# Kernel tuning notes

Measured on AMD Instinct MI355X. Metric: run time of the kernel, lower is better.

Reference implementation:

```python
import jax, jax.numpy as jnp
import numpy as np

EPS = 1e-15
N_NODES = 20000
N_EDGES = 640000
FEAT = 128
N_RBF = 20
CUTOFF = 5.0


def setup_inputs() -> dict:
    key = jax.random.key(0)
    ks = jax.random.split(key, 10)
    s_j = jax.random.normal(ks[0], (N_NODES, FEAT), jnp.float32)
    v_j = jax.random.normal(ks[1], (N_NODES, FEAT, 3), jnp.float32)
    r_ij = jax.random.normal(ks[2], (N_EDGES, 3), jnp.float32)
    nbrs = jax.random.randint(ks[3], (N_EDGES, 2), 0, N_NODES, jnp.int64)
    # InvariantDense: Dense(F->F, swish) then Dense(F->3F)
    W1 = jax.random.normal(ks[4], (FEAT, FEAT), jnp.float32) / np.sqrt(FEAT)
    b1 = jnp.zeros((FEAT,), jnp.float32)
    W2 = jax.random.normal(ks[5], (FEAT, 3 * FEAT), jnp.float32) / np.sqrt(FEAT)
    b2 = jnp.zeros((3 * FEAT,), jnp.float32)
    # DistanceEmbed dense: Dense(n_rbf -> 3F)
    Wd = jax.random.normal(ks[6], (N_RBF, 3 * FEAT), jnp.float32) / np.sqrt(N_RBF)
    bd = jnp.zeros((3 * FEAT,), jnp.float32)
    return {"s_j": s_j, "v_j": v_j, "r_ij": r_ij, "nbrs": nbrs,
            "W1": W1, "b1": b1, "W2": W2, "b2": b2, "Wd": Wd, "bd": bd}


def reference(s_j, v_j, r_ij, nbrs, W1, b1, W2, b2, Wd, bd):
    N, F = s_j.shape
    # preprocess_r
    dist = jnp.sqrt(jnp.sum(r_ij ** 2 + EPS, axis=-1))          # [E]
    unit = r_ij / dist[:, None]                                  # [E,3]
    # InvariantDense on nodes (dense before gather, as in torch code)
    phi_node = jax.nn.silu(s_j @ W1 + b1) @ W2 + b2              # [N,3F]
    phi = phi_node[nbrs[:, 1]]                                   # [E,3F]
    # PaiNN radial basis: sin(n*pi*d/cutoff)/d, n=1..n_rbf
    k = jnp.arange(1, N_RBF + 1, dtype=dist.dtype) * (np.pi / CUTOFF)  # [n_rbf]
    rbf = jnp.sin(dist[:, None] * k[None, :]) / dist[:, None]    # [E,n_rbf]
    # cosine cutoff envelope
    env = 0.5 * (jnp.cos(np.pi * dist / CUTOFF) + 1.0)
    env = jnp.where(dist < CUTOFF, env, 0.0)                     # [E]
    w_s = (rbf @ Wd + bd) * env[:, None]                         # [E,3F]
    inv = (phi * w_s).reshape(-1, 3, F)                          # [E,3,F]
    split0 = inv[:, 0, :][:, :, None]                            # [E,F,1]
    split1 = inv[:, 1, :]                                        # [E,F]
    split2 = inv[:, 2, :][:, :, None]                            # [E,F,1]
    delta_v_ij = split2 * unit[:, None, :] + split0 * v_j[nbrs[:, 1]]  # [E,F,3]
    idx = nbrs[:, 0]
    delta_s_i = jax.ops.segment_sum(split1, idx, num_segments=N)      # [N,F]
    delta_v_i = jax.ops.segment_sum(delta_v_ij, idx, num_segments=N)  # [N,F,3]
    return (delta_s_i, delta_v_i)
```

## Files before the change

kernel.cpp:

```cpp
#include <hip/hip_runtime.h>
#include <hip/hip_bf16.h>
#include <math.h>

typedef __hip_bfloat16 bf16;

#define FEAT 128
#define NRBF 20
#define CUTOFF_F 5.0f
#define KSCALE 0.62831853071795864769f

__device__ __forceinline__ float b2f(bf16 x) { return __bfloat162float(x); }
__device__ __forceinline__ bf16 f2b(float x) { return __float2bfloat16(x); }

template<int F32>
__device__ __forceinline__ float LD(const void* p, size_t i) {
    if (F32) return ((const float*)p)[i];
    return b2f(((const bf16*)p)[i]);
}
template<int F32>
__device__ __forceinline__ void ST(void* p, size_t i, float v) {
    if (F32) ((float*)p)[i] = v;
    else ((bf16*)p)[i] = f2b(v);
}

__device__ __forceinline__ int get_dst(const int* nb, int e, int is64) {
    return is64 ? nb[4 * e] : nb[2 * e];
}
__device__ __forceinline__ int get_src(const int* nb, int e, int is64) {
    return is64 ? nb[4 * e + 2] : nb[2 * e + 1];
}
__device__ __forceinline__ int clampi(int v, int n) {
    return v < 0 ? 0 : (v >= n ? n - 1 : v);
}

__global__ void init_kernel(const void* __restrict__ s_ptr, const int* __restrict__ nbrs32,
                            int nE, int* __restrict__ flags, int* __restrict__ counts, int nN) {
    int t = blockIdx.x * blockDim.x + threadIdx.x;
    if (t < nN) counts[t] = 0;
    if (t == 0) {
        const unsigned* u = (const unsigned*)s_ptr;
        int hits = 0;
        for (int i = 0; i < 64; ++i) {
            unsigned ef = (u[i] >> 7) & 0xFF;
            hits += (ef >= 110 && ef <= 135) ? 1 : 0;
        }
        flags[0] = (hits < 32) ? 1 : 0;
        int lim = 2 * nE; if (lim > 128) lim = 128;
        int allz = 1;
        for (int i = 1; i < lim; i += 2) allz &= (nbrs32[i] == 0);
        flags[1] = allz;
    }
}

__global__ void hist_kernel(const int* __restrict__ nbrs, const int* __restrict__ flags,
                            int* __restrict__ counts, int nE, int nN) {
    int e = blockIdx.x * blockDim.x + threadIdx.x;
    if (e < nE) {
        int d = clampi(get_dst(nbrs, e, flags[1]), nN);
        atomicAdd(&counts[d], 1);
    }
}

__global__ __launch_bounds__(1024) void scan_kernel(const int* __restrict__ counts,
        int* __restrict__ offsets, int* __restrict__ cursor, int nN) {
    __shared__ int part[1024];
    const int t = threadIdx.x;
    const int chunk = (nN + 1023) / 1024;
    const int base = t * chunk;
    int local[32];
    int sum = 0;
    for (int c = 0; c < chunk && c < 32; ++c) {
        int idx = base + c;
        int v = (idx < nN) ? counts[idx] : 0;
        local[c] = v;
        sum += v;
    }
    part[t] = sum;
    __syncthreads();
    for (int off = 1; off < 1024; off <<= 1) {
        int add = (t >= off) ? part[t - off] : 0;
        __syncthreads();
        part[t] += add;
        __syncthreads();
    }
    int run = part[t] - sum;
    for (int c = 0; c < chunk && c < 32; ++c) {
        int idx = base + c;
        if (idx < nN) { offsets[idx] = run; cursor[idx] = run; run += local[c]; }
    }
    if (t == 1023) offsets[nN] = part[1023];
}

__global__ __launch_bounds__(384) void prep_kernel(const void* __restrict__ Wd,
        const void* __restrict__ bd, float* __restrict__ WdT, const int* __restrict__ flags) {
    const int c = threadIdx.x;
    const int F32 = flags[0];
    if (F32) {
        for (int k = 0; k < NRBF; ++k) WdT[c * 24 + k] = ((const float*)Wd)[k * 384 + c];
        WdT[c * 24 + 20] = ((const float*)bd)[c];
    } else {
        for (int k = 0; k < NRBF; ++k) WdT[c * 24 + k] = b2f(((const bf16*)Wd)[k * 384 + c]);
        WdT[c * 24 + 20] = b2f(((const bf16*)bd)[c]);
    }
    WdT[c * 24 + 21] = 0.f; WdT[c * 24 + 22] = 0.f; WdT[c * 24 + 23] = 0.f;
}

template<int F32, int MODEA>
__device__ void pre_scatter_body(const void* __restrict__ r_ij, const int* __restrict__ nbrs,
        int is64, int* __restrict__ cursor, int* __restrict__ src_ids,
        float4* __restrict__ u_env, int* __restrict__ pos_of_e, float* __restrict__ gbuf,
        int e, int nE, int nN) {
    const int d = clampi(get_dst(nbrs, e, is64), nN);
    const int j = clampi(get_src(nbrs, e, is64), nN);
    int pos = atomicAdd(&cursor[d], 1);
    pos = clampi(pos, nE);
    src_ids[pos] = j;

    const float rx = LD<F32>(r_ij, (size_t)3 * e + 0);
    const float ry = LD<F32>(r_ij, (size_t)3 * e + 1);
    const float rz = LD<F32>(r_ij, (size_t)3 * e + 2);
    const float d2   = rx * rx + ry * ry + rz * rz + 3e-15f;
    const float invd = rsqrtf(d2);
    const float dd   = d2 * invd;
    const float x  = dd * KSCALE;
    const float c1 = F32 ? cosf(x) : __cosf(x);
    const float env = (dd < CUTOFF_F) ? (0.5f * (c1 + 1.0f)) : 0.0f;
    u_env[pos] = make_float4(rx * invd, ry * invd, rz * invd, env);

    if (MODEA) {
        pos_of_e[e] = pos;
    } else {
        const float s1 = F32 ? sinf(x) : __sinf(x);
        const float scale = invd * env;
        const float tc = 2.0f * c1;
        float skm2 = 0.f, skm1 = s1;
        float* g = gbuf + (size_t)pos * NRBF;
        g[0] = s1 * scale;
        #pragma unroll
        for (int k = 1; k < NRBF; ++k) {
            const float sk = fmaf(tc, skm1, -skm2);
            g[k] = sk * scale;
            skm2 = skm1; skm1 = sk;
        }
    }
}

__global__ __launch_bounds__(256) void pre_scatter_kernel(const void* r_ij, const int* nbrs,
        const int* __restrict__ flags, int* cursor, int* src_ids, float4* u_env,
        int* pos_of_e, float* gbuf, int nE, int nN, int modeA) {
    int e = blockIdx.x * blockDim.x + threadIdx.x;
    if (e >= nE) return;
    const int F32 = flags[0], is64 = flags[1];
    if (modeA) {
        if (F32) pre_scatter_body<1,1>(r_ij, nbrs, is64, cursor, src_ids, u_env, pos_of_e, gbuf, e, nE, nN);
        else     pre_scatter_body<0,1>(r_ij, nbrs, is64, cursor, src_ids, u_env, pos_of_e, gbuf, e, nE, nN);
    } else {
        if (F32) pre_scatter_body<1,0>(r_ij, nbrs, is64, cursor, src_ids, u_env, pos_of_e, gbuf, e, nE, nN);
        else     pre_scatter_body<0,0>(r_ij, nbrs, is64, cursor, src_ids, u_env, pos_of_e, gbuf, e, nE, nN);
    }
}

template<int F32>
__device__ void gemm_body(const void* __restrict__ s_j, const void* __restrict__ W1,
                          const void* __restrict__ b1, const void* __restrict__ W2,
                          const void* __restrict__ b2v, bf16* __restrict__ phi, int nN,
                          int packed) {
    __shared__ float sl[8][FEAT];
    __shared__ float hl[8][FEAT];
    const int t = threadIdx.x;
    const int n0 = blockIdx.x * 8;
    for (int idx = t; idx < 8 * FEAT; idx += 384) {
        int n = idx >> 7, k = idx & 127;
        int row = n0 + n;
        sl[n][k] = (row < nN) ? LD<F32>(s_j, (size_t)row * FEAT + k) : 0.f;
    }
    __syncthreads();
    for (int idx = t; idx < 8 * FEAT; idx += 384) {
        int n = idx >> 7, f = idx & 127;
        float a = 0.f;
        #pragma unroll 4
        for (int k = 0; k < FEAT; ++k) a = fmaf(sl[n][k], LD<F32>(W1, (size_t)k * FEAT + f), a);
        a += LD<F32>(b1, f);
        float sg = F32 ? (1.0f / (1.0f + expf(-a))) : (1.0f / (1.0f + __expf(-a)));
        hl[n][f] = a * sg;
    }
    __syncthreads();
    float acc[8] = {};
    #pragma unroll 4
    for (int k = 0; k < FEAT; ++k) {
        const float w = LD<F32>(W2, (size_t)k * 384 + t);
        #pragma unroll
        for (int n = 0; n < 8; ++n) acc[n] = fmaf(hl[n][k], w, acc[n]);
    }
    const float bb = LD<F32>(b2v, t);
    const int fch  = t & 127;
    const int comp = t >> 7;
    #pragma unroll
    for (int n = 0; n < 8; ++n) {
        int row = n0 + n;
        if (row < nN) {
            if (packed) phi[((size_t)row * FEAT + fch) * 8 + comp] = f2b(acc[n] + bb);
            else        phi[(size_t)row * 384 + t] = f2b(acc[n] + bb);
        }
    }
}

__global__ __launch_bounds__(384) void gemm_node_kernel(const void* s_j, const void* W1,
        const void* b1, const void* W2, const void* b2v, bf16* phi,
        const int* __restrict__ flags, int nN, int packed) {
    if (flags[0]) gemm_body<1>(s_j, W1, b1, W2, b2v, phi, nN, packed);
    else          gemm_body<0>(s_j, W1, b1, W2, b2v, phi, nN, packed);
}

__global__ __launch_bounds__(256) void pack_v_kernel(const void* __restrict__ v_j,
        bf16* __restrict__ rec, const int* __restrict__ flags, int nN) {
    int t = blockIdx.x * blockDim.x + threadIdx.x;
    if (t >= nN * FEAT) return;
    float vx, vy, vz;
    if (flags[0]) {
        const float* v = (const float*)v_j;
        vx = v[(size_t)3 * t + 0];
        vy = v[(size_t)3 * t + 1];
        vz = v[(size_t)3 * t + 2];
    } else {
        const bf16* v = (const bf16*)v_j;
        vx = b2f(v[(size_t)3 * t + 0]);
        vy = b2f(v[(size_t)3 * t + 1]);
        vz = b2f(v[(size_t)3 * t + 2]);
    }
    bf16* d = rec + (size_t)t * 8;
    union { bf16 b[2]; unsigned u; } p01;
    p01.b[0] = f2b(vx); p01.b[1] = f2b(vy);
    *(unsigned*)(d + 4) = p01.u;
    d[6] = f2b(vz);
}

template<int F32>
__device__ void pre_ws_body(const void* __restrict__ r_ij, const float* __restrict__ WdT,
        const int* __restrict__ pos_of_e, bf16* __restrict__ ws_w, int e) {
    const float rx = LD<F32>(r_ij, (size_t)3 * e + 0);
    const float ry = LD<F32>(r_ij, (size_t)3 * e + 1);
    const float rz = LD<F32>(r_ij, (size_t)3 * e + 2);
    const float d2   = rx * rx + ry * ry + rz * rz + 3e-15f;
    const float invd = rsqrtf(d2);
    const float dd   = d2 * invd;
    const float x  = dd * KSCALE;
    const float s1 = F32 ? sinf(x) : __sinf(x);
    const float c1 = F32 ? cosf(x) : __cosf(x);
    const float env = (dd < CUTOFF_F) ? (0.5f * (c1 + 1.0f)) : 0.0f;
    const float scale = invd * env;
    float gk[NRBF];
    const float tc = 2.0f * c1;
    float skm2 = 0.f, skm1 = s1;
    gk[0] = s1 * scale;
    #pragma unroll
    for (int k = 1; k < NRBF; ++k) {
        const float sk = fmaf(tc, skm1, -skm2);
        gk[k] = sk * scale;
        skm2 = skm1; skm1 = sk;
    }
    const int pos = pos_of_e[e];
    bf16* dst = ws_w + (size_t)pos * 384;
    for (int c0 = 0; c0 < 384; c0 += 4) {
        float r[4];
        #pragma unroll
        for (int u = 0; u < 4; ++u) {
            const float* w = WdT + (size_t)(c0 + u) * 24;
            float acc = w[20] * env;
            #pragma unroll
            for (int k = 0; k < NRBF; ++k) acc = fmaf(gk[k], w[k], acc);
            r[u] = acc;
        }
        union { bf16 b[4]; uint2 u2; } pk;
        pk.b[0] = f2b(r[0]); pk.b[1] = f2b(r[1]); pk.b[2] = f2b(r[2]); pk.b[3] = f2b(r[3]);
        *(uint2*)(dst + c0) = pk.u2;
    }
}

__global__ __launch_bounds__(256) void pre_ws_kernel(const void* r_ij,
        const float* __restrict__ WdT, const int* __restrict__ pos_of_e,
        bf16* __restrict__ ws_w, const int* __restrict__ flags, int nE) {
    int e = blockIdx.x * blockDim.x + threadIdx.x;
    if (e >= nE) return;
    if (flags[0]) pre_ws_body<1>(r_ij, WdT, pos_of_e, ws_w, e);
    else          pre_ws_body<0>(r_ij, WdT, pos_of_e, ws_w, e);
}

template<int F32>
__device__ void msg_a_body(const bf16* __restrict__ ws_w, const bf16* __restrict__ phi,
        const void* __restrict__ v_j, const int* __restrict__ src_ids,
        const float4* __restrict__ u_env, const int* __restrict__ offsets,
        void* __restrict__ out, int nE, int nN) {
    const int i = blockIdx.x;
    const int f = threadIdx.x;
    int start = offsets[i];
    int end   = offsets[i + 1];
    if (start < 0) start = 0;
    if (end > nE) end = nE;

    float ds = 0.f, dv0 = 0.f, dv1 = 0.f, dv2 = 0.f;

    #pragma unroll 2
    for (int p = start; p < end; ++p) {
        const int j = src_ids[p];
        const float4 ue = u_env[p];
        const bf16* wr = ws_w + (size_t)p * 384;
        const float w0 = b2f(wr[f]);
        const float w1 = b2f(wr[FEAT + f]);
        const float w2 = b2f(wr[2 * FEAT + f]);
        const bf16* ph = phi + (size_t)j * 384;
        const float p0 = b2f(ph[f]);
        const float p1 = b2f(ph[FEAT + f]);
        const float p2 = b2f(ph[2 * FEAT + f]);
        const float vx = LD<F32>(v_j, ((size_t)j * FEAT + f) * 3 + 0);
        const float vy = LD<F32>(v_j, ((size_t)j * FEAT + f) * 3 + 1);
        const float vz = LD<F32>(v_j, ((size_t)j * FEAT + f) * 3 + 2);
        const float i0 = w0 * p0;
        const float i1 = w1 * p1;
        const float i2 = w2 * p2;
        ds += i1;
        dv0 = fmaf(i2, ue.x, fmaf(i0, vx, dv0));
        dv1 = fmaf(i2, ue.y, fmaf(i0, vy, dv1));
        dv2 = fmaf(i2, ue.z, fmaf(i0, vz, dv2));
    }

    ST<F32>(out, (size_t)i * FEAT + f, ds);
    const size_t ob = (size_t)nN * FEAT + ((size_t)i * FEAT + f) * 3;
    ST<F32>(out, ob + 0, dv0);
    ST<F32>(out, ob + 1, dv1);
    ST<F32>(out, ob + 2, dv2);
}

__global__ __launch_bounds__(128) void msg_a_kernel(const bf16* ws_w, const bf16* phi,
        const void* v_j, const int* src_ids, const float4* u_env, const int* offsets,
        const int* __restrict__ flags, void* out, int nE, int nN) {
    if (flags[0]) msg_a_body<1>(ws_w, phi, v_j, src_ids, u_env, offsets, out, nE, nN);
    else          msg_a_body<0>(ws_w, phi, v_j, src_ids, u_env, offsets, out, nE, nN);
}

template<int F32>
__device__ void msg_c_body(const float* __restrict__ WdT, const bf16* __restrict__ rec,
        const float* __restrict__ gbuf, const int* __restrict__ src_ids,
        const float4* __restrict__ u_env, const int* __restrict__ offsets,
        void* __restrict__ out, int nE, int nN) {
    const int i = blockIdx.x;
    const int f = threadIdx.x;
    int start = offsets[i];
    int end   = offsets[i + 1];
    if (start < 0) start = 0;
    if (end > nE) end = nE;

    const float* w0p = WdT + (size_t)f * 24;
    const float* w1p = WdT + (size_t)(f + FEAT) * 24;
    const float* w2p = WdT + (size_t)(f + 2 * FEAT) * 24;

    float ds = 0.f, dv0 = 0.f, dv1 = 0.f, dv2 = 0.f;

    for (int p = start; p < end; ++p) {
        const int j = src_ids[p];
        const float4 ue = u_env[p];
        const float* g = gbuf + (size_t)p * NRBF;
        float t0 = 0.f, t1 = 0.f, t2 = 0.f;
        #pragma unroll
        for (int k = 0; k < NRBF; ++k) {
            const float gk = g[k];
            t0 = fmaf(gk, w0p[k], t0);
            t1 = fmaf(gk, w1p[k], t1);
            t2 = fmaf(gk, w2p[k], t2);
        }
        const float w0 = fmaf(w0p[20], ue.w, t0);
        const float w1 = fmaf(w1p[20], ue.w, t1);
        const float w2 = fmaf(w2p[20], ue.w, t2);

        const uint4 rv = *(const uint4*)(rec + ((size_t)j * FEAT + f) * 8);
        const float p0 = __uint_as_float(rv.x << 16);
        const float p1 = __uint_as_float(rv.x & 0xffff0000u);
        const float p2 = __uint_as_float(rv.y << 16);
        const float vx = __uint_as_float(rv.z << 16);
        const float vy = __uint_as_float(rv.z & 0xffff0000u);
        const float vz = __uint_as_float(rv.w << 16);

        const float i0 = w0 * p0;
        const float i1 = w1 * p1;
        const float i2 = w2 * p2;
        ds += i1;
        dv0 = fmaf(i2, ue.x, fmaf(i0, vx, dv0));
        dv1 = fmaf(i2, ue.y, fmaf(i0, vy, dv1));
        dv2 = fmaf(i2, ue.z, fmaf(i0, vz, dv2));
    }

    ST<F32>(out, (size_t)i * FEAT + f, ds);
    const size_t ob = (size_t)nN * FEAT + ((size_t)i * FEAT + f) * 3;
    ST<F32>(out, ob + 0, dv0);
    ST<F32>(out, ob + 1, dv1);
    ST<F32>(out, ob + 2, dv2);
}

__global__ __launch_bounds__(128) void msg_c_kernel(const float* WdT, const bf16* rec,
        const float* gbuf, const int* src_ids, const float4* u_env, const int* offsets,
        const int* __restrict__ flags, void* out, int nE, int nN) {
    if (flags[0]) msg_c_body<1>(WdT, rec, gbuf, src_ids, u_env, offsets, out, nE, nN);
    else          msg_c_body<0>(WdT, rec, gbuf, src_ids, u_env, offsets, out, nE, nN);
}

template<int F32>
__device__ void msg_b_body(const void* __restrict__ v_j, const void* __restrict__ Wd,
        const void* __restrict__ bd, const bf16* __restrict__ phi,
        const float* __restrict__ gbuf, const int* __restrict__ src_ids,
        const float4* __restrict__ u_env, const int* __restrict__ offsets,
        void* __restrict__ out, int nE, int nN) {
    const int i = blockIdx.x;
    const int f = threadIdx.x;

    float wd0[NRBF], wd1[NRBF], wd2[NRBF];
    #pragma unroll
    for (int k = 0; k < NRBF; ++k) {
        wd0[k] = LD<F32>(Wd, (size_t)k * 384 + f);
        wd1[k] = LD<F32>(Wd, (size_t)k * 384 + FEAT + f);
        wd2[k] = LD<F32>(Wd, (size_t)k * 384 + 2 * FEAT + f);
    }
    const float bd0 = LD<F32>(bd, f);
    const float bd1 = LD<F32>(bd, FEAT + f);
    const float bd2 = LD<F32>(bd, 2 * FEAT + f);

    int start = offsets[i];
    int end   = offsets[i + 1];
    if (start < 0) start = 0;
    if (end > nE) end = nE;

    float ds = 0.f, dv0 = 0.f, dv1 = 0.f, dv2 = 0.f;

    for (int p = start; p < end; ++p) {
        const int j = src_ids[p];
        const float4 ue = u_env[p];
        const float* g = gbuf + (size_t)p * NRBF;
        float t0 = 0.f, t1 = 0.f, t2 = 0.f;
        #pragma unroll
        for (int k = 0; k < NRBF; ++k) {
            const float gk = g[k];
            t0 = fmaf(gk, wd0[k], t0);
            t1 = fmaf(gk, wd1[k], t1);
            t2 = fmaf(gk, wd2[k], t2);
        }
        const float w0 = fmaf(bd0, ue.w, t0);
        const float w1 = fmaf(bd1, ue.w, t1);
        const float w2 = fmaf(bd2, ue.w, t2);

        const bf16* ph = phi + (size_t)j * 384;
        const float p0 = b2f(ph[f]);
        const float p1 = b2f(ph[FEAT + f]);
        const float p2 = b2f(ph[2 * FEAT + f]);
        const float vx = LD<F32>(v_j, ((size_t)j * FEAT + f) * 3 + 0);
        const float vy = LD<F32>(v_j, ((size_t)j * FEAT + f) * 3 + 1);
        const float vz = LD<F32>(v_j, ((size_t)j * FEAT + f) * 3 + 2);

        const float i0 = w0 * p0;
        const float i1 = w1 * p1;
        const float i2 = w2 * p2;
        ds += i1;
        dv0 = fmaf(i2, ue.x, fmaf(i0, vx, dv0));
        dv1 = fmaf(i2, ue.y, fmaf(i0, vy, dv1));
        dv2 = fmaf(i2, ue.z, fmaf(i0, vz, dv2));
    }

    ST<F32>(out, (size_t)i * FEAT + f, ds);
    const size_t ob = (size_t)nN * FEAT + ((size_t)i * FEAT + f) * 3;
    ST<F32>(out, ob + 0, dv0);
    ST<F32>(out, ob + 1, dv1);
    ST<F32>(out, ob + 2, dv2);
}

__global__ __launch_bounds__(128) void msg_b_kernel(const void* v_j, const void* Wd,
        const void* bd, const bf16* phi, const float* gbuf, const int* src_ids,
        const float4* u_env, const int* offsets, const int* __restrict__ flags,
        void* out, int nE, int nN) {
    if (flags[0]) msg_b_body<1>(v_j, Wd, bd, phi, gbuf, src_ids, u_env, offsets, out, nE, nN);
    else          msg_b_body<0>(v_j, Wd, bd, phi, gbuf, src_ids, u_env, offsets, out, nE, nN);
}

extern "C" void kernel_launch(void* const* d_in, const int* in_sizes, int n_in,
                              void* d_out, int out_size, void* d_ws, size_t ws_size,
                              hipStream_t stream) {
    const void* s_j  = d_in[0];
    const void* v_j  = d_in[1];
    const void* r_ij = d_in[2];
    const int*  nbrs = (const int*)d_in[3];
    const void* W1   = d_in[4];
    const void* b1   = d_in[5];
    const void* W2   = d_in[6];
    const void* b2   = d_in[7];
    const void* Wd   = d_in[8];
    const void* bd   = d_in[9];

    const int nN = out_size / (4 * FEAT);
    const int nE = in_sizes[2] / 3;

    char* ws = (char*)d_ws;
    size_t off = 0;
    auto alloc = [&](size_t bytes) -> void* {
        void* p = ws + off;
        off = (off + bytes + 255) & ~(size_t)255;
        return p;
    };
    int*    flags    = (int*)alloc(16);
    int*    counts   = (int*)alloc((size_t)nN * 4);
    int*    offsets  = (int*)alloc(((size_t)nN + 1) * 4);
    int*    cursor   = (int*)alloc((size_t)nN * 4);
    int*    src_ids  = (int*)alloc((size_t)nE * 4);
    float4* u_env    = (float4*)alloc((size_t)nE * 16);
    float*  WdT      = (float*)alloc((size_t)384 * 24 * 4);
    const size_t base = off;

    size_t offA = base;
    int*  pos_of_e = (int*)(ws + offA);  offA += ((size_t)nE * 4 + 255) & ~(size_t)255;
    bf16* phiA     = (bf16*)(ws + offA); offA += ((size_t)nN * 384 * 2 + 255) & ~(size_t)255;
    bf16* ws_w     = (bf16*)(ws + offA); offA += (size_t)nE * 384 * 2;
    size_t offC = base;
    float* gbufC = (float*)(ws + offC);  offC += ((size_t)nE * NRBF * 4 + 255) & ~(size_t)255;
    bf16*  rec   = (bf16*)(ws + offC);   offC += (size_t)nN * FEAT * 8 * 2;
    size_t offB = base;
    float* gbufB = (float*)(ws + offB);  offB += ((size_t)nE * NRBF * 4 + 255) & ~(size_t)255;
    bf16*  phiB  = (bf16*)(ws + offB);   offB += (size_t)nN * 384 * 2;

    const int modeA = (ws_size >= offA) ? 1 : 0;
    const int modeC = (!modeA && ws_size >= offC) ? 1 : 0;

    init_kernel<<<(nN + 255) / 256, 256, 0, stream>>>(s_j, nbrs, nE, flags, counts, nN);
    hist_kernel<<<(nE + 255) / 256, 256, 0, stream>>>(nbrs, flags, counts, nE, nN);
    scan_kernel<<<1, 1024, 0, stream>>>(counts, offsets, cursor, nN);
    prep_kernel<<<1, 384, 0, stream>>>(Wd, bd, WdT, flags);

    pre_scatter_kernel<<<(nE + 255) / 256, 256, 0, stream>>>(
        r_ij, nbrs, flags, cursor, src_ids, u_env, pos_of_e, gbufC, nE, nN, modeA);

    if (modeA) {
        gemm_node_kernel<<<(nN + 7) / 8, 384, 0, stream>>>(s_j, W1, b1, W2, b2, phiA, flags, nN, 0);
        pre_ws_kernel<<<(nE + 255) / 256, 256, 0, stream>>>(r_ij, WdT, pos_of_e, ws_w, flags, nE);
        msg_a_kernel<<<nN, 128, 0, stream>>>(ws_w, phiA, v_j, src_ids, u_env, offsets,
                                             flags, d_out, nE, nN);
    } else if (modeC) {
        gemm_node_kernel<<<(nN + 7) / 8, 384, 0, stream>>>(s_j, W1, b1, W2, b2, rec, flags, nN, 1);
        pack_v_kernel<<<((nN * FEAT) + 255) / 256, 256, 0, stream>>>(v_j, rec, flags, nN);
        msg_c_kernel<<<nN, 128, 0, stream>>>(WdT, rec, gbufC, src_ids, u_env, offsets,
                                             flags, d_out, nE, nN);
    } else {
        gemm_node_kernel<<<(nN + 7) / 8, 384, 0, stream>>>(s_j, W1, b1, W2, b2, phiB, flags, nN, 0);
        msg_b_kernel<<<nN, 128, 0, stream>>>(v_j, Wd, bd, phiB, gbufC, src_ids, u_env,
                                             offsets, flags, d_out, nE, nN);
    }
}
```

Measured before the change: 546.6 us.

## Split scatter into index pass and sorted-order RBF finalize; preload Wd in registers

In mode C the scatter pass now records only the source id and the original edge index for each sorted position. A new finalize kernel walks positions in sorted order and computes u_env and the RBF vector, writing them with contiguous float4 stores instead of scattered 80-byte writes. The message kernel loads its Wd rows into registers once and reads gbuf as float4, with launch bounds set to 128 threads and 2 blocks. The cost is an extra kernel launch, a gathered read of r_ij, and an extra nE-sized index buffer in the workspace, which may change which mode is selected.

After: 559.7 us. +2.4%, slower.

```diff
diff --git a/kernel.cpp b/kernel.cpp
--- a/kernel.cpp
+++ b/kernel.cpp
@@ -105,16 +105,21 @@
     WdT[c * 24 + 21] = 0.f; WdT[c * 24 + 22] = 0.f; WdT[c * 24 + 23] = 0.f;
 }
 
-template<int F32, int MODEA>
+template<int F32, int MODE>
 __device__ void pre_scatter_body(const void* __restrict__ r_ij, const int* __restrict__ nbrs,
         int is64, int* __restrict__ cursor, int* __restrict__ src_ids,
         float4* __restrict__ u_env, int* __restrict__ pos_of_e, float* __restrict__ gbuf,
-        int e, int nE, int nN) {
+        int* __restrict__ edge_of_pos, int e, int nE, int nN) {
     const int d = clampi(get_dst(nbrs, e, is64), nN);
     const int j = clampi(get_src(nbrs, e, is64), nN);
     int pos = atomicAdd(&cursor[d], 1);
     pos = clampi(pos, nE);
     src_ids[pos] = j;
+
+    if (MODE == 2) {
+        edge_of_pos[pos] = e;
+        return;
+    }
 
     const float rx = LD<F32>(r_ij, (size_t)3 * e + 0);
     const float ry = LD<F32>(r_ij, (size_t)3 * e + 1);
@@ -127,7 +132,7 @@
     const float env = (dd < CUTOFF_F) ? (0.5f * (c1 + 1.0f)) : 0.0f;
     u_env[pos] = make_float4(rx * invd, ry * invd, rz * invd, env);
 
-    if (MODEA) {
+    if (MODE == 1) {
         pos_of_e[e] = pos;
     } else {
         const float s1 = F32 ? sinf(x) : __sinf(x);
@@ -147,17 +152,62 @@
 
 __global__ __launch_bounds__(256) void pre_scatter_kernel(const void* r_ij, const int* nbrs,
         const int* __restrict__ flags, int* cursor, int* src_ids, float4* u_env,
-        int* pos_of_e, float* gbuf, int nE, int nN, int modeA) {
+        int* pos_of_e, float* gbuf, int* edge_of_pos, int nE, int nN, int mode) {
     int e = blockIdx.x * blockDim.x + threadIdx.x;
     if (e >= nE) return;
     const int F32 = flags[0], is64 = flags[1];
-    if (modeA) {
-        if (F32) pre_scatter_body<1,1>(r_ij, nbrs, is64, cursor, src_ids, u_env, pos_of_e, gbuf, e, nE, nN);
-        else     pre_scatter_body<0,1>(r_ij, nbrs, is64, cursor, src_ids, u_env, pos_of_e, gbuf, e, nE, nN);
+    if (mode == 2) {
+        if (F32) pre_scatter_body<1,2>(r_ij, nbrs, is64, cursor, src_ids, u_env, pos_of_e, gbuf, edge_of_pos, e, nE, nN);
+        else     pre_scatter_body<0,2>(r_ij, nbrs, is64, cursor, src_ids, u_env, pos_of_e, gbuf, edge_of_pos, e, nE, nN);
+    } else if (mode == 1) {
+        if (F32) pre_scatter_body<1,1>(r_ij, nbrs, is64, cursor, src_ids, u_env, pos_of_e, gbuf, edge_of_pos, e, nE, nN);
+        else     pre_scatter_body<0,1>(r_ij, nbrs, is64, cursor, src_ids, u_env, pos_of_e, gbuf, edge_of_pos, e, nE, nN);
     } else {
-        if (F32) pre_scatter_body<1,0>(r_ij, nbrs, is64, cursor, src_ids, u_env, pos_of_e, gbuf, e, nE, nN);
-        else     pre_scatter_body<0,0>(r_ij, nbrs, is64, cursor, src_ids, u_env, pos_of_e, gbuf, e, nE, nN);
-    }
+        if (F32) pre_scatter_body<1,0>(r_ij, nbrs, is64, cursor, src_ids, u_env, pos_of_e, gbuf, edge_of_pos, e, nE, nN);
+        else     pre_scatter_body<0,0>(r_ij, nbrs, is64, cursor, src_ids, u_env, pos_of_e, gbuf, edge_of_pos, e, nE, nN);
+    }
+}
+
+template<int F32>
+__device__ void finalize_body(const void* __restrict__ r_ij, const int* __restrict__ edge_of_pos,
+        float4* __restrict__ u_env, float* __restrict__ gbuf, int t, int nE) {
+    const int e = clampi(edge_of_pos[t], nE);
+    const float rx = LD<F32>(r_ij, (size_t)3 * e + 0);
+    const float ry = LD<F32>(r_ij, (size_t)3 * e + 1);
+    const float rz = LD<F32>(r_ij, (size_t)3 * e + 2);
+    const float d2   = rx * rx + ry * ry + rz * rz + 3e-15f;
+    const float invd = rsqrtf(d2);
+    const float dd   = d2 * invd;
+    const float x  = dd * KSCALE;
+    const float c1 = F32 ? cosf(x) : __cosf(x);
+    const float s1 = F32 ? sinf(x) : __sinf(x);
+    const float env = (dd < CUTOFF_F) ? (0.5f * (c1 + 1.0f)) : 0.0f;
+    u_env[t] = make_float4(rx * invd, ry * invd, rz * invd, env);
+
+    const float scale = invd * env;
+    const float tc = 2.0f * c1;
+    float g[NRBF];
+    float skm2 = 0.f, skm1 = s1;
+    g[0] = s1 * scale;
+    #pragma unroll
+    for (int k = 1; k < NRBF; ++k) {
+        const float sk = fmaf(tc, skm1, -skm2);
+        g[k] = sk * scale;
+        skm2 = skm1; skm1 = sk;
+    }
+    float4* gd = (float4*)(gbuf + (size_t)t * NRBF);
+    #pragma unroll
+    for (int q = 0; q < 5; ++q)
+        gd[q] = make_float4(g[4*q], g[4*q+1], g[4*q+2], g[4*q+3]);
+}
+
+__global__ __launch_bounds__(256) void finalize_kernel(const void* r_ij,
+        const int* __restrict__ edge_of_pos, float4* __restrict__ u_env,
+        float* __restrict__ gbuf, const int* __restrict__ flags, int nE) {
+    int t = blockIdx.x * blockDim.x + threadIdx.x;
+    if (t >= nE) return;
+    if (flags[0]) finalize_body<1>(r_ij, edge_of_pos, u_env, gbuf, t, nE);
+    else          finalize_body<0>(r_ij, edge_of_pos, u_env, gbuf, t, nE);
 }
 
 template<int F32>
@@ -350,27 +400,36 @@
     if (start < 0) start = 0;
     if (end > nE) end = nE;
 
-    const float* w0p = WdT + (size_t)f * 24;
-    const float* w1p = WdT + (size_t)(f + FEAT) * 24;
-    const float* w2p = WdT + (size_t)(f + 2 * FEAT) * 24;
+    const float4* wq0 = (const float4*)(WdT + (size_t)f * 24);
+    const float4* wq1 = (const float4*)(WdT + (size_t)(f + FEAT) * 24);
+    const float4* wq2 = (const float4*)(WdT + (size_t)(f + 2 * FEAT) * 24);
+    float4 A0[5], A1[5], A2[5];
+    #pragma unroll
+    for (int q = 0; q < 5; ++q) { A0[q] = wq0[q]; A1[q] = wq1[q]; A2[q] = wq2[q]; }
+    const float B0 = WdT[(size_t)f * 24 + 20];
+    const float B1 = WdT[(size_t)(f + FEAT) * 24 + 20];
+    const float B2 = WdT[(size_t)(f + 2 * FEAT) * 24 + 20];
 
     float ds = 0.f, dv0 = 0.f, dv1 = 0.f, dv2 = 0.f;
 
     for (int p = start; p < end; ++p) {
         const int j = src_ids[p];
         const float4 ue = u_env[p];
-        const float* g = gbuf + (size_t)p * NRBF;
+        const float4* g4 = (const float4*)(gbuf + (size_t)p * NRBF);
         float t0 = 0.f, t1 = 0.f, t2 = 0.f;
         #pragma unroll
-        for (int k = 0; k < NRBF; ++k) {
-            const float gk = g[k];
-            t0 = fmaf(gk, w0p[k], t0);
-            t1 = fmaf(gk, w1p[k], t1);
-            t2 = fmaf(gk, w2p[k], t2);
+        for (int q = 0; q < 5; ++q) {
+            const float4 gq = g4[q];
+            t0 = fmaf(gq.x, A0[q].x, t0); t0 = fmaf(gq.y, A0[q].y, t0);
+            t0 = fmaf(gq.z, A0[q].z, t0); t0 = fmaf(gq.w, A0[q].w, t0);
+            t1 = fmaf(gq.x, A1[q].x, t1); t1 = fmaf(gq.y, A1[q].y, t1);
+            t1 = fmaf(gq.z, A1[q].z, t1); t1 = fmaf(gq.w, A1[q].w, t1);
+            t2 = fmaf(gq.x, A2[q].x, t2); t2 = fmaf(gq.y, A2[q].y, t2);
+            t2 = fmaf(gq.z, A2[q].z, t2); t2 = fmaf(gq.w, A2[q].w, t2);
         }
-        const float w0 = fmaf(w0p[20], ue.w, t0);
-        const float w1 = fmaf(w1p[20], ue.w, t1);
-        const float w2 = fmaf(w2p[20], ue.w, t2);
+        const float w0 = fmaf(B0, ue.w, t0);
+        const float w1 = fmaf(B1, ue.w, t1);
+        const float w2 = fmaf(B2, ue.w, t2);
 
         const uint4 rv = *(const uint4*)(rec + ((size_t)j * FEAT + f) * 8);
         const float p0 = __uint_as_float(rv.x << 16);
@@ -396,7 +455,7 @@
     ST<F32>(out, ob + 2, dv2);
 }
 
-__global__ __launch_bounds__(128) void msg_c_kernel(const float* WdT, const bf16* rec,
+__global__ __launch_bounds__(128, 2) void msg_c_kernel(const float* WdT, const bf16* rec,
         const float* gbuf, const int* src_ids, const float4* u_env, const int* offsets,
         const int* __restrict__ flags, void* out, int nE, int nN) {
     if (flags[0]) msg_c_body<1>(WdT, rec, gbuf, src_ids, u_env, offsets, out, nE, nN);
@@ -517,7 +576,8 @@
     bf16* ws_w     = (bf16*)(ws + offA); offA += (size_t)nE * 384 * 2;
     size_t offC = base;
     float* gbufC = (float*)(ws + offC);  offC += ((size_t)nE * NRBF * 4 + 255) & ~(size_t)255;
-    bf16*  rec   = (bf16*)(ws + offC);   offC += (size_t)nN * FEAT * 8 * 2;
+    bf16*  rec   = (bf16*)(ws + offC);   offC += ((size_t)nN * FEAT * 8 * 2 + 255) & ~(size_t)255;
+    int* edge_of_pos = (int*)(ws + offC); offC += (size_t)nE * 4;
     size_t offB = base;
     float* gbufB = (float*)(ws + offB);  offB += ((size_t)nE * NRBF * 4 + 255) & ~(size_t)255;
     bf16*  phiB  = (bf16*)(ws + offB);   offB += (size_t)nN * 384 * 2;
@@ -530,8 +590,10 @@
     scan_kernel<<<1, 1024, 0, stream>>>(counts, offsets, cursor, nN);
     prep_kernel<<<1, 384, 0, stream>>>(Wd, bd, WdT, flags);
 
+    const int psMode = modeA ? 1 : (modeC ? 2 : 0);
     pre_scatter_kernel<<<(nE + 255) / 256, 256, 0, stream>>>(
-        r_ij, nbrs, flags, cursor, src_ids, u_env, pos_of_e, gbufC, nE, nN, modeA);
+        r_ij, nbrs, flags, cursor, src_ids, u_env, pos_of_e, gbufC, edge_of_pos,
+        nE, nN, psMode);
 
     if (modeA) {
         gemm_node_kernel<<<(nN + 7) / 8, 384, 0, stream>>>(s_j, W1, b1, W2, b2, phiA, flags, nN, 0);
@@ -539,6 +601,8 @@
         msg_a_kernel<<<nN, 128, 0, stream>>>(ws_w, phiA, v_j, src_ids, u_env, offsets,
                                              flags, d_out, nE, nN);
     } else if (modeC) {
+        finalize_kernel<<<(nE + 255) / 256, 256, 0, stream>>>(r_ij, edge_of_pos, u_env,
+                                                              gbufC, flags, nE);
         gemm_node_kernel<<<(nN + 7) / 8, 384, 0, stream>>>(s_j, W1, b1, W2, b2, rec, flags, nN, 1);
         pack_v_kernel<<<((nN * FEAT) + 255) / 256, 256, 0, stream>>>(v_j, rec, flags, nN);
         msg_c_kernel<<<nN, 128, 0, stream>>>(WdT, rec, gbufC, src_ids, u_env, offsets,
```
